# Optimization experiments

Measured on AMD Instinct MI355X. Metric: run time of the kernel, lower is better.

The kernel has to match this reference:

```python
import jax, jax.numpy as jnp
import numpy as np

_OFFS = np.array([(dx, dy, dz) for dx in (-1, 0, 1) for dy in (-1, 0, 1) for dz in (-1, 0, 1)], np.int64)


def setup_inputs() -> dict:
    rng = np.random.default_rng(0)
    B, G, NPTS = 2, 128, 100000
    # level-0 active voxel coords (batch, x, y, z)
    cs = []
    for b in range(B):
        xyz = np.unique(rng.integers(0, G, size=(NPTS, 3)), axis=0)
        cs.append(np.concatenate([np.full((len(xyz), 1), b, np.int64), xyz], 1))
    c0 = np.concatenate(cs, 0)
    c1 = np.unique(np.concatenate([c0[:, :1], c0[:, 1:] // 2], 1), axis=0)  # stride-2 coords
    c2 = np.unique(np.concatenate([c1[:, :1], c1[:, 1:] // 2], 1), axis=0)  # stride-4 coords

    def table(c, g):  # dense coordinate hash: coord -> row index, -1 if empty
        t = np.full((B, g, g, g), -1, np.int64)
        t[c[:, 0], c[:, 1], c[:, 2], c[:, 3]] = np.arange(len(c))
        return t

    t0, t1, t2 = table(c0, G), table(c1, G // 2), table(c2, G // 4)

    def kmap(out_c, tab, g, stride):  # kernel map for k=3 conv: [27, Nout], -1 = no neighbor
        base = out_c[:, 1:] * stride
        nbr = np.empty((27, len(out_c)), np.int32)
        for k, off in enumerate(_OFFS):
            p = base + off
            ok = ((p >= 0) & (p < g)).all(1)
            pc = np.clip(p, 0, g - 1)
            nbr[k] = np.where(ok, tab[out_c[:, 0], pc[:, 0], pc[:, 1], pc[:, 2]], -1)
        return nbr

    nbr0 = kmap(c0, t0, G, 1)        # enc1: submanifold, out coords == in coords
    nbr1 = kmap(c1, t0, G, 2)        # enc2: stride-2 downsample
    nbr2 = kmap(c2, t1, G // 2, 2)   # enc3: stride-2 downsample

    def upmap(fine_c, coarse_tab):   # k=2 s=2 transposed conv: unique parent + offset id
        q = fine_c[:, 1:] // 2
        idx = coarse_tab[fine_c[:, 0], q[:, 0], q[:, 1], q[:, 2]].astype(np.int32)
        r = fine_c[:, 1:] - 2 * q
        off = (r[:, 0] * 4 + r[:, 1] * 2 + r[:, 2]).astype(np.int32)
        return idx, off

    up1_idx, up1_off = upmap(c1, t2)  # dec2: level2 -> level1
    up0_idx, up0_off = upmap(c0, t1)  # dec1: level1 -> level0

    def w(shape):
        return jnp.asarray(rng.normal(0.0, 0.05, shape).astype(np.float32))

    feats = jnp.asarray(rng.normal(0.0, 1.0, (len(c0), 2)).astype(np.float32))
    return dict(
        feats=feats,
        W1=w((27, 2, 32)), W2=w((27, 32, 64)), W3=w((27, 64, 128)),
        W4=w((8, 128, 64)), W5=w((8, 64, 32)), Wout=w((32, 2)),
        g1=jnp.ones(32), b1=jnp.zeros(32), g2=jnp.ones(64), b2=jnp.zeros(64),
        g3=jnp.ones(128), b3=jnp.zeros(128), g4=jnp.ones(64), b4=jnp.zeros(64),
        g5=jnp.ones(32), b5=jnp.zeros(32),
        nbr0=jnp.asarray(nbr0), nbr1=jnp.asarray(nbr1), nbr2=jnp.asarray(nbr2),
        up1_idx=jnp.asarray(up1_idx), up1_off=jnp.asarray(up1_off),
        up0_idx=jnp.asarray(up0_idx), up0_off=jnp.asarray(up0_off),
    )


def _sconv(f, nbr, W):
    # implicit-GEMM sparse conv: gather per kernel offset, matmul, masked accumulate
    out = jnp.zeros((nbr.shape[1], W.shape[2]), f.dtype)
    for k in range(W.shape[0]):
        idx = nbr[k]
        g = jnp.where((idx >= 0)[:, None], f[jnp.maximum(idx, 0)], 0.0)
        out = out + g @ W[k]
    return out


def _upconv(f, pidx, poff, W):
    # k=2 s=2 transposed conv: each fine voxel has exactly one coarse parent + offset id in [0,8)
    g = f[pidx]
    out = jnp.zeros((g.shape[0], W.shape[2]), f.dtype)
    for k in range(8):
        out = out + jnp.where((poff == k)[:, None], g @ W[k], 0.0)
    return out


def _bn_relu(x, g, b):
    # training-mode BatchNorm over the voxel dim (biased var), then ReLU
    mu = x.mean(0)
    var = x.var(0)
    return jax.nn.relu((x - mu) * jax.lax.rsqrt(var + 1e-5) * g + b)


def reference(feats, W1, W2, W3, W4, W5, Wout, g1, b1, g2, b2, g3, b3, g4, b4, g5, b5,
              nbr0, nbr1, nbr2, up1_idx, up1_off, up0_idx, up0_off):
    e1 = _bn_relu(_sconv(feats, nbr0, W1), g1, b1)   # [N0, 32]
    e2 = _bn_relu(_sconv(e1, nbr1, W2), g2, b2)      # [N1, 64]
    e3 = _bn_relu(_sconv(e2, nbr2, W3), g3, b3)      # [N2, 128]
    d2 = _bn_relu(_upconv(e3, up1_idx, up1_off, W4), g4, b4)  # [N1, 64]
    d1 = _bn_relu(_upconv(d2, up0_idx, up0_off, W5), g5, b5)  # [N0, 32]
    return d1 @ Wout                                  # 1x1 conv, [N0, 2]
```

## Files before the change

### kernel.cpp

```cpp
#include <hip/hip_runtime.h>
#include <hip/hip_bf16.h>

typedef __attribute__((ext_vector_type(4))) float  f32x4;
typedef __attribute__((ext_vector_type(8))) short  short8;
typedef __attribute__((ext_vector_type(2))) float  flt2;
typedef long long ll;

__device__ __forceinline__ short f2bf(float f) {
    __hip_bfloat16 h = __float2bfloat16(f);
    short s; __builtin_memcpy(&s, &h, 2);
    return s;
}
__device__ __forceinline__ float bf2f(short s) {
    unsigned u = ((unsigned)(unsigned short)s) << 16;
    float f; __builtin_memcpy(&f, &u, 4);
    return f;
}
__device__ __forceinline__ void gload_lds16(const void* g, void* l) {
    __builtin_amdgcn_global_load_lds(
        (const __attribute__((address_space(1))) unsigned*)(g),
        (__attribute__((address_space(3))) unsigned*)(l),
        16, 0, 0);
}

__global__ void prep_kernel(const float* __restrict__ W1, const float* __restrict__ W2,
                            const float* __restrict__ W3, const float* __restrict__ W4,
                            const float* __restrict__ W5,
                            short* W1t, short* W2t, short* W3t, short* W4t, short* W5t) {
    int gid = blockIdx.x * 256 + threadIdx.x;
    if (gid < 32 * 64) {
        int co = gid >> 6, e = gid & 63;
        float v = 0.f;
        if (e < 54) { int k = e >> 1, ci = e & 1; v = W1[(k * 2 + ci) * 32 + co]; }
        W1t[gid] = f2bf(v);
        return;
    }
    int g = gid - 32 * 64;
    if (g < 28 * 2048) { int k = g / 2048, r = g % 2048, co = r >> 5, ci = r & 31;
        W2t[g] = (k < 27) ? f2bf(W2[((ll)k * 32 + ci) * 64 + co]) : (short)0; return; }
    g -= 28 * 2048;
    if (g < 28 * 8192) { int k = g / 8192, r = g % 8192, co = r >> 6, ci = r & 63;
        W3t[g] = (k < 27) ? f2bf(W3[((ll)k * 64 + ci) * 128 + co]) : (short)0; return; }
    g -= 28 * 8192;
    if (g < 8 * 64 * 128) { int k = g / (64*128), r = g % (64*128), co = r >> 7, ci = r & 127;
        W4t[g] = f2bf(W4[((ll)k * 128 + ci) * 64 + co]); return; }
    g -= 8 * 64 * 128;
    if (g < 8 * 32 * 64) { int k = g / (32*64), r = g % (32*64), co = r >> 6, ci = r & 63;
        W5t[g] = f2bf(W5[((ll)k * 64 + ci) * 32 + co]); return; }
}

__launch_bounds__(256)
__global__ void c1_kernel(const float* __restrict__ feats, const int* __restrict__ nbr,
                          const short* __restrict__ W1t, short* __restrict__ out,
                          float* __restrict__ part, int N) {
    __shared__ float sc[8 * 32];
    int tid = threadIdx.x, lane = tid & 63, wave = tid >> 6;
    int rb = blockIdx.x * 64 + wave * 16;
    int r = rb + (lane & 15);
    int rl = r < N ? r : N - 1;
    int seg = lane >> 4, l15 = lane & 15;
    f32x4 acc[2];
    acc[0] = (f32x4){0,0,0,0}; acc[1] = (f32x4){0,0,0,0};
    short8 a[2];
    #pragma unroll
    for (int kc = 0; kc < 2; ++kc) {
        #pragma unroll
        for (int j = 0; j < 4; ++j) {
            int k = kc * 16 + seg * 4 + j;
            flt2 f = (flt2){0.f, 0.f};
            if (k < 27) {
                int idx = nbr[(ll)k * N + rl];
                if (idx >= 0) f = *(const flt2*)(feats + 2 * (ll)idx);
            }
            a[kc][2*j]   = f2bf(f[0]);
            a[kc][2*j+1] = f2bf(f[1]);
        }
    }
    #pragma unroll
    for (int kc = 0; kc < 2; ++kc)
        #pragma unroll
        for (int c = 0; c < 2; ++c) {
            short8 b = *(const short8*)(W1t + (c*16 + l15) * 64 + kc * 32 + seg * 8);
            acc[c] = __builtin_amdgcn_mfma_f32_16x16x32_bf16(a[kc], b, acc[c], 0, 0, 0);
        }
    int r0 = rb + seg * 4;
    #pragma unroll
    for (int c = 0; c < 2; ++c) {
        int col = c * 16 + l15;
        #pragma unroll
        for (int j = 0; j < 4; ++j)
            if (r0 + j < N) out[(ll)(r0 + j) * 32 + col] = f2bf(acc[c][j]);
    }
    float s[2], q[2];
    #pragma unroll
    for (int c = 0; c < 2; ++c) { s[c] = 0.f; q[c] = 0.f; }
    #pragma unroll
    for (int c = 0; c < 2; ++c)
        #pragma unroll
        for (int j = 0; j < 4; ++j) {
            float v = (r0 + j < N) ? acc[c][j] : 0.f;
            s[c] += v; q[c] += v * v;
        }
    #pragma unroll
    for (int c = 0; c < 2; ++c) {
        s[c] += __shfl_xor(s[c], 16); q[c] += __shfl_xor(q[c], 16);
        s[c] += __shfl_xor(s[c], 32); q[c] += __shfl_xor(q[c], 32);
    }
    if (lane < 16) {
        #pragma unroll
        for (int c = 0; c < 2; ++c) {
            sc[(wave * 2 + 0) * 32 + c * 16 + l15] = s[c];
            sc[(wave * 2 + 1) * 32 + c * 16 + l15] = q[c];
        }
    }
    __syncthreads();
    for (int i = tid; i < 32; i += 256) {
        float ss = sc[0*32+i] + sc[2*32+i] + sc[4*32+i] + sc[6*32+i];
        float qq = sc[1*32+i] + sc[3*32+i] + sc[5*32+i] + sc[7*32+i];
        part[(ll)blockIdx.x * 64 + i]      = ss;
        part[(ll)blockIdx.x * 64 + 32 + i] = qq;
    }
}

template<int CIN, int COLS, int RG, int MINW>
__launch_bounds__(256, MINW)
__global__ void msconv5_kernel(const short* __restrict__ inb, const int* __restrict__ nbr,
                               const short* __restrict__ Wt, short* __restrict__ out,
                               float* __restrict__ part, int N, int zoff) {
    constexpr int KC = CIN / 32, NT = COLS / 16;
    constexpr int CPK = COLS * CIN / 8, BIT = CPK / 256;
    constexpr int WST = COLS * CIN;
    constexpr int SH = (CIN == 32) ? 6 : 7;
    constexpr int P = RG + BIT + RG * KC;
    __shared__ __align__(16) short lb[3][WST];

    const int tid = threadIdx.x, lane = tid & 63, wave = tid >> 6;
    const int seg = lane >> 4, l15 = lane & 15;
    const int wrb = blockIdx.x * (64 * RG) + wave * (16 * RG);
    const char* inB = (const char*)inb;

    int rl[RG];
    #pragma unroll
    for (int rg = 0; rg < RG; ++rg) {
        int r = wrb + rg * 16 + l15;
        rl[rg] = r < N ? r : N - 1;
    }

    auto rawIdx = [&](int k, int (&ix)[RG]) {
        #pragma unroll
        for (int rg = 0; rg < RG; ++rg) ix[rg] = nbr[(ll)k * N + rl[rg]];
    };
    auto mkoff = [&](const int (&ix)[RG], int (&o)[RG]) {
        #pragma unroll
        for (int rg = 0; rg < RG; ++rg) o[rg] = (ix[rg] >= 0) ? (ix[rg] << SH) : zoff;
    };
    auto stage = [&](int kn, int buf) {
        #pragma unroll
        for (int it = 0; it < BIT; ++it) {
            int q = it * 256 + tid;
            int co = q % COLS, sg = (q / COLS) & 3, kc = q / (COLS * 4);
            gload_lds16(Wt + (ll)kn * WST + co * CIN + kc * 32 + sg * 8, &lb[buf][q * 8]);
        }
    };
    auto ldA = [&](short8 (&a)[RG][KC], const int (&o)[RG]) {
        #pragma unroll
        for (int rg = 0; rg < RG; ++rg) {
            const char* base = inB + o[rg];
            #pragma unroll
            for (int kc = 0; kc < KC; ++kc)
                a[rg][kc] = *(const short8*)(base + kc * 64 + seg * 16);
        }
    };

    f32x4 acc[RG][NT];
    #pragma unroll
    for (int rg = 0; rg < RG; ++rg)
        #pragma unroll
        for (int c = 0; c < NT; ++c) acc[rg][c] = (f32x4){0.f, 0.f, 0.f, 0.f};

    auto compute = [&](int buf, short8 (&a)[RG][KC]) {
        #pragma unroll
        for (int kc = 0; kc < KC; ++kc)
            #pragma unroll
            for (int c = 0; c < NT; ++c) {
                short8 b = *(const short8*)&lb[buf][((kc * 4 + seg) * COLS + c * 16 + l15) * 8];
                #pragma unroll
                for (int rg = 0; rg < RG; ++rg)
                    acc[rg][c] = __builtin_amdgcn_mfma_f32_16x16x32_bf16(
                        a[rg][kc], b, acc[rg][c], 0, 0, 0);
            }
    };

    short8 aA[RG][KC], aB[RG][KC];
    int iF[RG], offC[RG];

    {
        int i0[RG], i1[RG], o0[RG];
        rawIdx(0, i0); rawIdx(1, i1); rawIdx(2, iF);
        mkoff(i0, o0); mkoff(i1, offC);
        stage(0, 0); stage(1, 1);
        __builtin_amdgcn_sched_barrier(0);
        ldA(aA, o0);
        __builtin_amdgcn_sched_barrier(0);
        asm volatile("s_waitcnt vmcnt(%0) lgkmcnt(0)" :: "n"(BIT + RG * KC) : "memory");
        __builtin_amdgcn_s_barrier();
        __builtin_amdgcn_sched_barrier(0);
    }

    #pragma unroll
    for (int k = 0; k < 27; ++k) {
        int iN[RG];
        {
            int kq = (k + 3 < 27) ? (k + 3) : 26;
            rawIdx(kq, iN);
            int kt = (k + 2 < 27) ? (k + 2) : 27;
            stage(kt, (k + 2) % 3);
        }
        __builtin_amdgcn_sched_barrier(0);
        if (k & 1) ldA(aA, offC); else ldA(aB, offC);
        __builtin_amdgcn_sched_barrier(0);
        if (k & 1) compute(k % 3, aB); else compute(k % 3, aA);
        __builtin_amdgcn_sched_barrier(0);
        asm volatile("s_waitcnt vmcnt(%0) lgkmcnt(0)" :: "n"(P) : "memory");
        __builtin_amdgcn_s_barrier();
        __builtin_amdgcn_sched_barrier(0);
        mkoff(iF, offC);
        #pragma unroll
        for (int rg = 0; rg < RG; ++rg) iF[rg] = iN[rg];
    }

    #pragma unroll
    for (int rg = 0; rg < RG; ++rg)
        #pragma unroll
        for (int c = 0; c < NT; ++c) {
            int col = c * 16 + l15;
            #pragma unroll
            for (int j = 0; j < 4; ++j) {
                int rr = wrb + rg * 16 + seg * 4 + j;
                if (rr < N) out[(ll)rr * COLS + col] = f2bf(acc[rg][c][j]);
            }
        }

    float s[NT], q[NT];
    #pragma unroll
    for (int c = 0; c < NT; ++c) { s[c] = 0.f; q[c] = 0.f; }
    #pragma unroll
    for (int rg = 0; rg < RG; ++rg)
        #pragma unroll
        for (int c = 0; c < NT; ++c)
            #pragma unroll
            for (int j = 0; j < 4; ++j) {
                int rr = wrb + rg * 16 + seg * 4 + j;
                float v = (rr < N) ? acc[rg][c][j] : 0.f;
                s[c] += v; q[c] += v * v;
            }
    #pragma unroll
    for (int c = 0; c < NT; ++c) {
        s[c] += __shfl_xor(s[c], 16); q[c] += __shfl_xor(q[c], 16);
        s[c] += __shfl_xor(s[c], 32); q[c] += __shfl_xor(q[c], 32);
    }
    float* sc = (float*)&lb[0][0];
    if (lane < 16) {
        #pragma unroll
        for (int c = 0; c < NT; ++c) {
            sc[(wave * 2 + 0) * COLS + c * 16 + l15] = s[c];
            sc[(wave * 2 + 1) * COLS + c * 16 + l15] = q[c];
        }
    }
    __syncthreads();
    for (int i = tid; i < COLS; i += 256) {
        float ss = sc[0*COLS+i] + sc[2*COLS+i] + sc[4*COLS+i] + sc[6*COLS+i];
        float qq = sc[1*COLS+i] + sc[3*COLS+i] + sc[5*COLS+i] + sc[7*COLS+i];
        part[(ll)blockIdx.x * 2 * COLS + i]        = ss;
        part[(ll)blockIdx.x * 2 * COLS + COLS + i] = qq;
    }
}

__global__ void dcount_kernel(const int* __restrict__ poff, int* __restrict__ cnt, int N) {
    __shared__ int lc[8];
    if (threadIdx.x < 8) lc[threadIdx.x] = 0;
    __syncthreads();
    int r = blockIdx.x * 256 + threadIdx.x;
    if (r < N) atomicAdd(&lc[poff[r]], 1);
    __syncthreads();
    if (threadIdx.x < 8 && lc[threadIdx.x]) atomicAdd(&cnt[threadIdx.x], lc[threadIdx.x]);
}

__global__ void dprefix_kernel(const int* __restrict__ cnt, int* __restrict__ bases,
                               int* __restrict__ kofb, int* __restrict__ perm, int nblk) {
    __shared__ int base[9];
    if (threadIdx.x == 0) {
        int b = 0;
        for (int k = 0; k < 8; ++k) { base[k] = b; b += (cnt[k] + 63) & ~63; }
        base[8] = b;
        for (int k = 0; k < 9; ++k) bases[k] = base[k];
    }
    __syncthreads();
    int nb = base[8] >> 6;
    for (int i = threadIdx.x; i < nblk; i += 256) {
        int k = -1;
        if (i < nb) {
            int rb = i << 6; k = 0;
            while (rb >= base[k + 1]) ++k;
        }
        kofb[i] = k;
    }
    for (int k = 0; k < 8; ++k) {
        int s = base[k] + cnt[k], e = base[k + 1];
        for (int i = s + threadIdx.x; i < e; i += 256) perm[i] = -1;
    }
}

__global__ void dscatter_kernel(const int* __restrict__ poff, const int* __restrict__ bases,
                                int* __restrict__ cur, int* __restrict__ perm, int N) {
    __shared__ int lc[8], lbs[8];
    if (threadIdx.x < 8) lc[threadIdx.x] = 0;
    __syncthreads();
    int r = blockIdx.x * 256 + threadIdx.x;
    int k = 0, myl = 0;
    if (r < N) { k = poff[r]; myl = atomicAdd(&lc[k], 1); }
    __syncthreads();
    if (threadIdx.x < 8) lbs[threadIdx.x] = atomicAdd(&cur[threadIdx.x], lc[threadIdx.x]);
    __syncthreads();
    if (r < N) perm[bases[k] + lbs[k] + myl] = r;
}

template<int CIN, int COUT>
__launch_bounds__(256)
__global__ void gdec_kernel(const short* __restrict__ inb, const int* __restrict__ perm,
                            const int* __restrict__ kofb, const int* __restrict__ pidx,
                            const short* __restrict__ Wt, const short* __restrict__ zrow,
                            short* __restrict__ out, float* __restrict__ part) {
    constexpr int KC = CIN / 32, NT = COUT / 16;
    constexpr int CPK = COUT * CIN / 8, BIT = CPK / 256;
    __shared__ __align__(16) short lb[COUT * CIN];
    const int tid = threadIdx.x, lane = tid & 63, wave = tid >> 6;
    int k = kofb[blockIdx.x];
    if (k < 0) {
        for (int i = tid; i < 2 * COUT; i += 256) part[(ll)blockIdx.x * 2 * COUT + i] = 0.f;
        return;
    }
    const int seg = lane >> 4, l15 = lane & 15;
    const int wrb = blockIdx.x * 64 + wave * 16;
    int rl = wrb + l15;
    int pr = perm[rl];
    int idx = pr < 0 ? -1 : pidx[pr];

    #pragma unroll
    for (int it = 0; it < BIT; ++it) {
        int q = it * 256 + tid;
        int co = q % COUT, sg = (q / COUT) & 3, kc = q / (COUT * 4);
        gload_lds16(Wt + ((ll)k * COUT + co) * CIN + kc * 32 + sg * 8, &lb[q * 8]);
    }
    short8 a[KC];
    const short* base = (idx < 0) ? zrow : (inb + (ll)idx * CIN);
    #pragma unroll
    for (int kc = 0; kc < KC; ++kc)
        a[kc] = *(const short8*)(base + kc * 32 + seg * 8);

    f32x4 acc[NT];
    #pragma unroll
    for (int c = 0; c < NT; ++c) acc[c] = (f32x4){0.f, 0.f, 0.f, 0.f};
    __syncthreads();
    #pragma unroll
    for (int kc = 0; kc < KC; ++kc)
        #pragma unroll
        for (int c = 0; c < NT; ++c) {
            short8 b = *(const short8*)&lb[((kc * 4 + seg) * COUT + c * 16 + l15) * 8];
            acc[c] = __builtin_amdgcn_mfma_f32_16x16x32_bf16(a[kc], b, acc[c], 0, 0, 0);
        }
    #pragma unroll
    for (int j = 0; j < 4; ++j) {
        int prs = __shfl(pr, seg * 4 + j, 64);
        if (prs >= 0) {
            #pragma unroll
            for (int c = 0; c < NT; ++c)
                out[(ll)prs * COUT + c * 16 + l15] = f2bf(acc[c][j]);
        }
    }
    float s[NT], q[NT];
    #pragma unroll
    for (int c = 0; c < NT; ++c) { s[c] = 0.f; q[c] = 0.f; }
    #pragma unroll
    for (int c = 0; c < NT; ++c)
        #pragma unroll
        for (int j = 0; j < 4; ++j) { float v = acc[c][j]; s[c] += v; q[c] += v * v; }
    #pragma unroll
    for (int c = 0; c < NT; ++c) {
        s[c] += __shfl_xor(s[c], 16); q[c] += __shfl_xor(q[c], 16);
        s[c] += __shfl_xor(s[c], 32); q[c] += __shfl_xor(q[c], 32);
    }
    __syncthreads();
    float* sc = (float*)lb;
    if (lane < 16) {
        #pragma unroll
        for (int c = 0; c < NT; ++c) {
            sc[(wave * 2 + 0) * COUT + c * 16 + l15] = s[c];
            sc[(wave * 2 + 1) * COUT + c * 16 + l15] = q[c];
        }
    }
    __syncthreads();
    for (int i = tid; i < COUT; i += 256) {
        float ss = sc[0*COUT+i] + sc[2*COUT+i] + sc[4*COUT+i] + sc[6*COUT+i];
        float qq = sc[1*COUT+i] + sc[3*COUT+i] + sc[5*COUT+i] + sc[7*COUT+i];
        part[(ll)blockIdx.x * 2 * COUT + i]        = ss;
        part[(ll)blockIdx.x * 2 * COUT + COUT + i] = qq;
    }
}

__global__ void red2_kernel(const float* __restrict__ part, int nblk,
                            const float* __restrict__ g, const float* __restrict__ bb,
                            float* __restrict__ A, float* __restrict__ B, int C, int N) {
    int c = blockIdx.x;
    float s = 0.f, q = 0.f;
    for (int i = threadIdx.x; i < nblk; i += 256) {
        s += part[(ll)i * 2 * C + c];
        q += part[(ll)i * 2 * C + C + c];
    }
    __shared__ float ls[256], lq[256];
    ls[threadIdx.x] = s; lq[threadIdx.x] = q;
    __syncthreads();
    for (int str = 128; str >= 1; str >>= 1) {
        if (threadIdx.x < str) {
            ls[threadIdx.x] += ls[threadIdx.x + str];
            lq[threadIdx.x] += lq[threadIdx.x + str];
        }
        __syncthreads();
    }
    if (threadIdx.x == 0) {
        float inv = 1.0f / (float)N;
        float mu = ls[0] * inv, var = lq[0] * inv - mu * mu;
        float a = g[c] * rsqrtf(var + 1e-5f);
        A[c] = a; B[c] = bb[c] - mu * a;
    }
}

template<int C>
__global__ void bnrelu_kernel(const short* __restrict__ x, const float* __restrict__ A,
                              const float* __restrict__ B, short* __restrict__ out, int N) {
    constexpr int CPR = C / 8;
    int i = blockIdx.x * 256 + threadIdx.x;
    if (i >= N * CPR) return;
    int r = i / CPR, ch = i - r * CPR;
    short8 v = *(const short8*)(x + (ll)r * C + ch * 8);
    short8 o;
    #pragma unroll
    for (int j = 0; j < 8; ++j) {
        int c = ch * 8 + j;
        float y = fmaf(bf2f(v[j]), A[c], B[c]);
        o[j] = f2bf(y > 0.f ? y : 0.f);
    }
    *(short8*)(out + (ll)r * C + ch * 8) = o;
}

__global__ void outk_kernel(const short* __restrict__ z, const float* __restrict__ A,
                            const float* __restrict__ B, const float* __restrict__ Wout,
                            float* __restrict__ out, int N) {
    __shared__ float w[64], sa[32], sb[32];
    if (threadIdx.x < 64) w[threadIdx.x] = Wout[threadIdx.x];
    if (threadIdx.x < 32) { sa[threadIdx.x] = A[threadIdx.x]; sb[threadIdx.x] = B[threadIdx.x]; }
    __syncthreads();
    int r = blockIdx.x * 256 + threadIdx.x;
    if (r >= N) return;
    const short* zp = z + (ll)r * 32;
    float o0 = 0.f, o1 = 0.f;
    #pragma unroll
    for (int s4 = 0; s4 < 4; ++s4) {
        short8 v = *(const short8*)(zp + s4 * 8);
        #pragma unroll
        for (int j = 0; j < 8; ++j) {
            int c = s4 * 8 + j;
            float y = fmaf(bf2f(v[j]), sa[c], sb[c]);
            y = y > 0.f ? y : 0.f;
            o0 = fmaf(y, w[2*c], o0);
            o1 = fmaf(y, w[2*c+1], o1);
        }
    }
    out[(ll)r * 2]     = o0;
    out[(ll)r * 2 + 1] = o1;
}

extern "C" void kernel_launch(void* const* d_in, const int* in_sizes, int n_in,
                              void* d_out, int out_size, void* d_ws, size_t ws_size,
                              hipStream_t stream) {
    const float* feats = (const float*)d_in[0];
    const float* W1 = (const float*)d_in[1];
    const float* W2 = (const float*)d_in[2];
    const float* W3 = (const float*)d_in[3];
    const float* W4 = (const float*)d_in[4];
    const float* W5 = (const float*)d_in[5];
    const float* Wout = (const float*)d_in[6];
    const float* g1 = (const float*)d_in[7],  *b1 = (const float*)d_in[8];
    const float* g2 = (const float*)d_in[9],  *b2 = (const float*)d_in[10];
    const float* g3 = (const float*)d_in[11], *b3 = (const float*)d_in[12];
    const float* g4 = (const float*)d_in[13], *b4 = (const float*)d_in[14];
    const float* g5 = (const float*)d_in[15], *b5 = (const float*)d_in[16];
    const int* nbr0 = (const int*)d_in[17];
    const int* nbr1 = (const int*)d_in[18];
    const int* nbr2 = (const int*)d_in[19];
    const int* up1_idx = (const int*)d_in[20];
    const int* up1_off = (const int*)d_in[21];
    const int* up0_idx = (const int*)d_in[22];
    const int* up0_off = (const int*)d_in[23];

    const int N0 = in_sizes[0] / 2;
    const int N1 = in_sizes[20];
    const int N2 = in_sizes[19] / 27;

    char* cur = (char*)d_ws;
    auto alloc = [&](size_t bytes) { char* p = cur; cur += (bytes + 255) & ~255ULL; return p; };
    auto cdiv = [](ll a, ll b) { return (int)((a + b - 1) / b); };

    float* stats = (float*)alloc(4096);
    float* A1 = stats,       *B1c = stats + 32;
    float* A2 = stats + 64,  *B2c = stats + 128;
    float* A3 = stats + 192, *B3c = stats + 320;
    float* A4 = stats + 448, *B4c = stats + 512;
    float* A5 = stats + 576, *B5c = stats + 608;
    short* zrow  = (short*)((char*)stats + 2560);
    int*   cnt4  = (int*)((char*)stats + 3072);
    int*   cur4  = (int*)((char*)stats + 3104);
    int*   cnt5  = (int*)((char*)stats + 3136);
    int*   cur5  = (int*)((char*)stats + 3168);
    int*   bas4  = (int*)((char*)stats + 3200);
    int*   bas5  = (int*)((char*)stats + 3264);

    float* part = (float*)alloc(2 * 1024 * 1024);

    size_t zmax = (size_t)N1 * 64;
    if ((size_t)N0 * 32  > zmax) zmax = (size_t)N0 * 32;
    if ((size_t)N2 * 128 > zmax) zmax = (size_t)N2 * 128;
    short* zb  = (short*)alloc(zmax * 2);
    short* e1b = (short*)alloc((size_t)N0 * 32 * 2);
    short* e2b = (short*)alloc((size_t)N1 * 64 * 2);
    short* e3b = (short*)alloc((size_t)N2 * 128 * 2);
    short* d2b = (short*)alloc((size_t)N1 * 64 * 2);
    short* W1t = (short*)alloc(32 * 64 * 2);
    short* W2t = (short*)alloc((size_t)28 * 64 * 32 * 2);
    short* W3t = (short*)alloc((size_t)28 * 128 * 64 * 2);
    short* W4t = (short*)alloc((size_t)8 * 64 * 128 * 2);
    short* W5t = (short*)alloc((size_t)8 * 32 * 64 * 2);

    const int gridL4 = cdiv((ll)N1 + 512, 64);
    const int gridL5 = cdiv((ll)N0 + 512, 64);
    int* perm4 = (int*)alloc((size_t)gridL4 * 64 * 4);
    int* kofb4 = (int*)alloc((size_t)gridL4 * 4);
    int* perm5 = (int*)alloc((size_t)gridL5 * 64 * 4);
    int* kofb5 = (int*)alloc((size_t)gridL5 * 4);

    const int zoff1 = (int)((ll)((char*)zrow - (char*)e1b));
    const int zoff2 = (int)((ll)((char*)zrow - (char*)e2b));

    const int nblk1 = cdiv(N0, 64);
    const int nblk2 = cdiv(N1, 128);
    const int nblk3 = cdiv(N2, 128);

    hipMemsetAsync((char*)stats + 2560, 0, 640, stream);

    prep_kernel<<<cdiv(2048 + 28*2048 + 28*8192 + 65536 + 16384, 256), 256, 0, stream>>>(
        W1, W2, W3, W4, W5, W1t, W2t, W3t, W4t, W5t);

    dcount_kernel<<<cdiv(N1, 256), 256, 0, stream>>>(up1_off, cnt4, N1);
    dprefix_kernel<<<1, 256, 0, stream>>>(cnt4, bas4, kofb4, perm4, gridL4);
    dscatter_kernel<<<cdiv(N1, 256), 256, 0, stream>>>(up1_off, bas4, cur4, perm4, N1);
    dcount_kernel<<<cdiv(N0, 256), 256, 0, stream>>>(up0_off, cnt5, N0);
    dprefix_kernel<<<1, 256, 0, stream>>>(cnt5, bas5, kofb5, perm5, gridL5);
    dscatter_kernel<<<cdiv(N0, 256), 256, 0, stream>>>(up0_off, bas5, cur5, perm5, N0);

    c1_kernel<<<nblk1, 256, 0, stream>>>(feats, nbr0, W1t, zb, part, N0);
    red2_kernel<<<32, 256, 0, stream>>>(part, nblk1, g1, b1, A1, B1c, 32, N0);
    bnrelu_kernel<32><<<cdiv((ll)N0 * 4, 256), 256, 0, stream>>>(zb, A1, B1c, e1b, N0);

    msconv5_kernel<32, 64, 2, 4><<<nblk2, 256, 0, stream>>>(e1b, nbr1, W2t, zb, part, N1, zoff1);
    red2_kernel<<<64, 256, 0, stream>>>(part, nblk2, g2, b2, A2, B2c, 64, N1);
    bnrelu_kernel<64><<<cdiv((ll)N1 * 8, 256), 256, 0, stream>>>(zb, A2, B2c, e2b, N1);

    msconv5_kernel<64, 128, 2, 3><<<nblk3, 256, 0, stream>>>(e2b, nbr2, W3t, zb, part, N2, zoff2);
    red2_kernel<<<128, 256, 0, stream>>>(part, nblk3, g3, b3, A3, B3c, 128, N2);
    bnrelu_kernel<128><<<cdiv((ll)N2 * 16, 256), 256, 0, stream>>>(zb, A3, B3c, e3b, N2);

    gdec_kernel<128, 64><<<gridL4, 256, 0, stream>>>(e3b, perm4, kofb4, up1_idx, W4t, zrow, zb, part);
    red2_kernel<<<64, 256, 0, stream>>>(part, gridL4, g4, b4, A4, B4c, 64, N1);
    bnrelu_kernel<64><<<cdiv((ll)N1 * 8, 256), 256, 0, stream>>>(zb, A4, B4c, d2b, N1);

    gdec_kernel<64, 32><<<gridL5, 256, 0, stream>>>(d2b, perm5, kofb5, up0_idx, W5t, zrow, zb, part);
    red2_kernel<<<32, 256, 0, stream>>>(part, gridL5, g5, b5, A5, B5c, 32, N0);
    outk_kernel<<<cdiv(N0, 256), 256, 0, stream>>>(zb, A5, B5c, Wout, (float*)d_out, N0);
}
```

Baseline: 259.8 us.

## Process kernel offsets in pairs with double-buffered LDS weight staging

The sparse conv kernel now handles two kernel offsets per pipeline step: 14 iterations instead of 27, LDS weights double-buffered in pairs instead of triple-buffered singly, and gathered activations loaded for two offsets at once. This halves the number of block barriers and waitcnt stalls per block and gives each wave more independent loads in flight. The cost is more registers and more LDS, so the enc3 launch drops its min-waves hint from 3 to 2, lowering occupancy. For the 27th offset it reads a 28th weight slice, which relies on padding in the prepared weight buffer.

```diff
diff --git a/kernel.cpp b/kernel.cpp
--- a/kernel.cpp
+++ b/kernel.cpp
@@ -124,15 +124,14 @@
 
 template<int CIN, int COLS, int RG, int MINW>
 __launch_bounds__(256, MINW)
-__global__ void msconv5_kernel(const short* __restrict__ inb, const int* __restrict__ nbr,
+__global__ void msconv6_kernel(const short* __restrict__ inb, const int* __restrict__ nbr,
                                const short* __restrict__ Wt, short* __restrict__ out,
                                float* __restrict__ part, int N, int zoff) {
     constexpr int KC = CIN / 32, NT = COLS / 16;
     constexpr int CPK = COLS * CIN / 8, BIT = CPK / 256;
     constexpr int WST = COLS * CIN;
     constexpr int SH = (CIN == 32) ? 6 : 7;
-    constexpr int P = RG + BIT + RG * KC;
-    __shared__ __align__(16) short lb[3][WST];
+    __shared__ __align__(16) short lb[2][2 * WST];
 
     const int tid = threadIdx.x, lane = tid & 63, wave = tid >> 6;
     const int seg = lane >> 4, l15 = lane & 15;
@@ -146,87 +145,104 @@
         rl[rg] = r < N ? r : N - 1;
     }
 
-    auto rawIdx = [&](int k, int (&ix)[RG]) {
-        #pragma unroll
-        for (int rg = 0; rg < RG; ++rg) ix[rg] = nbr[(ll)k * N + rl[rg]];
+    auto rawIdx2 = [&](int p, int (&ix)[2][RG]) {
+        #pragma unroll
+        for (int kk = 0; kk < 2; ++kk) {
+            int kq = 2 * p + kk; if (kq > 26) kq = 26;
+            #pragma unroll
+            for (int rg = 0; rg < RG; ++rg) ix[kk][rg] = nbr[(ll)kq * N + rl[rg]];
+        }
     };
-    auto mkoff = [&](const int (&ix)[RG], int (&o)[RG]) {
-        #pragma unroll
-        for (int rg = 0; rg < RG; ++rg) o[rg] = (ix[rg] >= 0) ? (ix[rg] << SH) : zoff;
+    auto mkoff2 = [&](const int (&ix)[2][RG], int (&o)[2][RG]) {
+        #pragma unroll
+        for (int kk = 0; kk < 2; ++kk)
+            #pragma unroll
+            for (int rg = 0; rg < RG; ++rg)
+                o[kk][rg] = (ix[kk][rg] >= 0) ? (ix[kk][rg] << SH) : zoff;
     };
-    auto stage = [&](int kn, int buf) {
-        #pragma unroll
-        for (int it = 0; it < BIT; ++it) {
-            int q = it * 256 + tid;
-            int co = q % COLS, sg = (q / COLS) & 3, kc = q / (COLS * 4);
-            gload_lds16(Wt + (ll)kn * WST + co * CIN + kc * 32 + sg * 8, &lb[buf][q * 8]);
-        }
-    };
-    auto ldA = [&](short8 (&a)[RG][KC], const int (&o)[RG]) {
-        #pragma unroll
-        for (int rg = 0; rg < RG; ++rg) {
-            const char* base = inB + o[rg];
-            #pragma unroll
-            for (int kc = 0; kc < KC; ++kc)
-                a[rg][kc] = *(const short8*)(base + kc * 64 + seg * 16);
-        }
-    };
-
-    f32x4 acc[RG][NT];
-    #pragma unroll
-    for (int rg = 0; rg < RG; ++rg)
-        #pragma unroll
-        for (int c = 0; c < NT; ++c) acc[rg][c] = (f32x4){0.f, 0.f, 0.f, 0.f};
-
-    auto compute = [&](int buf, short8 (&a)[RG][KC]) {
-        #pragma unroll
-        for (int kc = 0; kc < KC; ++kc)
-            #pragma unroll
-            for (int c = 0; c < NT; ++c) {
-                short8 b = *(const short8*)&lb[buf][((kc * 4 + seg) * COLS + c * 16 + l15) * 8];
-                #pragma unroll
-                for (int rg = 0; rg < RG; ++rg)
-                    acc[rg][c] = __builtin_amdgcn_mfma_f32_16x16x32_bf16(
-                        a[rg][kc], b, acc[rg][c], 0, 0, 0);
+    auto stage2 = [&](int p, int buf) {
+        #pragma unroll
+        for (int kk = 0; kk < 2; ++kk)
+            #pragma unroll
+            for (int it = 0; it < BIT; ++it) {
+                int q = it * 256 + tid;
+                int co = q % COLS, sg = (q / COLS) & 3, kc = q / (COLS * 4);
+                gload_lds16(Wt + (ll)(2 * p + kk) * WST + co * CIN + kc * 32 + sg * 8,
+                            &lb[buf][kk * WST + q * 8]);
             }
     };
-
-    short8 aA[RG][KC], aB[RG][KC];
-    int iF[RG], offC[RG];
+    auto ldA2 = [&](short8 (&a)[2][RG][KC], const int (&o)[2][RG]) {
+        #pragma unroll
+        for (int kk = 0; kk < 2; ++kk)
+            #pragma unroll
+            for (int rg = 0; rg < RG; ++rg) {
+                const char* base = inB + o[kk][rg];
+                #pragma unroll
+                for (int kc = 0; kc < KC; ++kc)
+                    a[kk][rg][kc] = *(const short8*)(base + kc * 64 + seg * 16);
+            }
+    };
+
+    f32x4 acc[RG][NT];
+    #pragma unroll
+    for (int rg = 0; rg < RG; ++rg)
+        #pragma unroll
+        for (int c = 0; c < NT; ++c) acc[rg][c] = (f32x4){0.f, 0.f, 0.f, 0.f};
+
+    auto compute2 = [&](int buf, short8 (&a)[2][RG][KC]) {
+        #pragma unroll
+        for (int kk = 0; kk < 2; ++kk)
+            #pragma unroll
+            for (int kc = 0; kc < KC; ++kc)
+                #pragma unroll
+                for (int c = 0; c < NT; ++c) {
+                    short8 b = *(const short8*)&lb[buf][kk * WST
+                                + ((kc * 4 + seg) * COLS + c * 16 + l15) * 8];
+                    #pragma unroll
+                    for (int rg = 0; rg < RG; ++rg)
+                        acc[rg][c] = __builtin_amdgcn_mfma_f32_16x16x32_bf16(
+                            a[kk][rg][kc], b, acc[rg][c], 0, 0, 0);
+                }
+    };
+
+    short8 aA[2][RG][KC], aB[2][RG][KC];
+    int iF[2][RG], offC[2][RG];
 
     {
-        int i0[RG], i1[RG], o0[RG];
-        rawIdx(0, i0); rawIdx(1, i1); rawIdx(2, iF);
-        mkoff(i0, o0); mkoff(i1, offC);
-        stage(0, 0); stage(1, 1);
+        int i0[2][RG], i1[2][RG], o0[2][RG];
+        rawIdx2(0, i0); rawIdx2(1, i1); rawIdx2(2, iF);
+        mkoff2(i0, o0); mkoff2(i1, offC);
+        stage2(0, 0);
         __builtin_amdgcn_sched_barrier(0);
-        ldA(aA, o0);
+        ldA2(aA, o0);
         __builtin_amdgcn_sched_barrier(0);
-        asm volatile("s_waitcnt vmcnt(%0) lgkmcnt(0)" :: "n"(BIT + RG * KC) : "memory");
+        asm volatile("s_waitcnt vmcnt(%0) lgkmcnt(0)" :: "n"(2 * RG * KC) : "memory");
         __builtin_amdgcn_s_barrier();
         __builtin_amdgcn_sched_barrier(0);
     }
 
     #pragma unroll
-    for (int k = 0; k < 27; ++k) {
-        int iN[RG];
+    for (int p = 0; p < 14; ++p) {
+        int iN[2][RG];
         {
-            int kq = (k + 3 < 27) ? (k + 3) : 26;
-            rawIdx(kq, iN);
-            int kt = (k + 2 < 27) ? (k + 2) : 27;
-            stage(kt, (k + 2) % 3);
+            int pq = (p + 3 < 14) ? (p + 3) : 13;
+            rawIdx2(pq, iN);
+            int ps = (p + 1 < 14) ? (p + 1) : 13;
+            stage2(ps, (p + 1) & 1);
         }
         __builtin_amdgcn_sched_barrier(0);
-        if (k & 1) ldA(aA, offC); else ldA(aB, offC);
+        if (p & 1) ldA2(aA, offC); else ldA2(aB, offC);
         __builtin_amdgcn_sched_barrier(0);
-        if (k & 1) compute(k % 3, aB); else compute(k % 3, aA);
+        if (p & 1) compute2(1, aB); else compute2(0, aA);
         __builtin_amdgcn_sched_barrier(0);
-        asm volatile("s_waitcnt vmcnt(%0) lgkmcnt(0)" :: "n"(P) : "memory");
+        asm volatile("s_waitcnt vmcnt(%0) lgkmcnt(0)" :: "n"(2 * RG * KC) : "memory");
         __builtin_amdgcn_s_barrier();
         __builtin_amdgcn_sched_barrier(0);
-        mkoff(iF, offC);
-        #pragma unroll
-        for (int rg = 0; rg < RG; ++rg) iF[rg] = iN[rg];
+        mkoff2(iF, offC);
+        #pragma unroll
+        for (int kk = 0; kk < 2; ++kk)
+            #pragma unroll
+            for (int rg = 0; rg < RG; ++rg) iF[kk][rg] = iN[kk][rg];
     }
 
     #pragma unroll
@@ -571,11 +587,11 @@
     red2_kernel<<<32, 256, 0, stream>>>(part, nblk1, g1, b1, A1, B1c, 32, N0);
     bnrelu_kernel<32><<<cdiv((ll)N0 * 4, 256), 256, 0, stream>>>(zb, A1, B1c, e1b, N0);
 
-    msconv5_kernel<32, 64, 2, 4><<<nblk2, 256, 0, stream>>>(e1b, nbr1, W2t, zb, part, N1, zoff1);
+    msconv6_kernel<32, 64, 2, 4><<<nblk2, 256, 0, stream>>>(e1b, nbr1, W2t, zb, part, N1, zoff1);
     red2_kernel<<<64, 256, 0, stream>>>(part, nblk2, g2, b2, A2, B2c, 64, N1);
     bnrelu_kernel<64><<<cdiv((ll)N1 * 8, 256), 256, 0, stream>>>(zb, A2, B2c, e2b, N1);
 
-    msconv5_kernel<64, 128, 2, 3><<<nblk3, 256, 0, stream>>>(e2b, nbr2, W3t, zb, part, N2, zoff2);
+    msconv6_kernel<64, 128, 2, 2><<<nblk3, 256, 0, stream>>>(e2b, nbr2, W3t, zb, part, N2, zoff2);
     red2_kernel<<<128, 256, 0, stream>>>(part, nblk3, g3, b3, A3, B3c, 128, N2);
     bnrelu_kernel<128><<<cdiv((ll)N2 * 16, 256), 256, 0, stream>>>(zb, A3, B3c, e3b, N2);
 
```

New measurement: 260.9 us. Within noise of the previous version (+0.4%).
